# Kernel optimization log

Hardware: AMD Instinct MI355X
Metric: run time of the kernel (lower is better)

The kernel has to match this reference:

```python
import jax, jax.numpy as jnp
import numpy as np

NUM_HEAD = 16


def setup_inputs() -> dict:
    key = jax.random.key(0)
    ks = jax.random.split(key, 7)
    B, S, E = 2, 2048, 1024
    scale = 0.02
    return {
        "x": jax.random.normal(ks[0], (B, S, E), dtype=jnp.float32),
        "Wq": jax.random.normal(ks[1], (E, E), dtype=jnp.float32) * scale,
        "bq": jax.random.normal(ks[2], (E,), dtype=jnp.float32) * scale,
        "Wk": jax.random.normal(ks[3], (E, E), dtype=jnp.float32) * scale,
        "bk": jax.random.normal(ks[4], (E,), dtype=jnp.float32) * scale,
        "Wv": jax.random.normal(ks[5], (E, E), dtype=jnp.float32) * scale,
        "bv": jax.random.normal(ks[6], (E,), dtype=jnp.float32) * scale,
    }


def reference(x, Wq, bq, Wk, bk, Wv, bv):
    B, S, E = x.shape
    H = NUM_HEAD
    Dh = E // H
    # torch Linear: y = x @ W.T + b
    q = (x @ Wq.T + bq).reshape(B, S, H, Dh).transpose(0, 2, 1, 3)  # [B,H,S,Dh]
    k = (x @ Wk.T + bk).reshape(B, S, H, Dh).transpose(0, 2, 1, 3)
    v = (x @ Wv.T + bv).reshape(B, S, H, Dh).transpose(0, 2, 1, 3)
    attn = jnp.einsum("bhqd,bhkd->bhqk", q, k) / jnp.sqrt(jnp.float32(Dh))
    score = jax.nn.softmax(attn, axis=-1)
    out = jnp.einsum("bhqk,bhkd->bhqd", score, v)  # [B,H,S,Dh]
    return out.transpose(0, 2, 1, 3).reshape(B, S, E)
```

## Files before the change

### kernel.cpp

```cpp
#include <hip/hip_runtime.h>
#include <hip/hip_bf16.h>
#include <stdint.h>

#define S_LEN 2048
#define E_DIM 1024
#define NHEAD 16
#define DHEAD 64
#define BATCH 2

typedef short bf16x8 __attribute__((ext_vector_type(8)));
typedef float f32x4 __attribute__((ext_vector_type(4)));
typedef float f32x16 __attribute__((ext_vector_type(16)));

__device__ __forceinline__ ushort f2bf(float f) {
    uint32_t u = __builtin_bit_cast(uint32_t, f);
    u += 0x7fffu + ((u >> 16) & 1u);
    return (ushort)(u >> 16);
}
__device__ __forceinline__ float bf2f(ushort h) {
    uint32_t u = ((uint32_t)h) << 16;
    return __builtin_bit_cast(float, u);
}
__device__ __forceinline__ uint32_t packbf2(float a, float b) {
    return (uint32_t)f2bf(a) | ((uint32_t)f2bf(b) << 16);
}
__device__ __forceinline__ f32x16 zero16() {
    f32x16 v;
    #pragma unroll
    for (int i = 0; i < 16; ++i) v[i] = 0.f;
    return v;
}

__global__ __launch_bounds__(256) void convert_kernel(
    const float* __restrict__ x, const float* __restrict__ wq,
    const float* __restrict__ wk, const float* __restrict__ wv,
    ushort* __restrict__ xb, ushort* __restrict__ wqb,
    ushort* __restrict__ wkb, ushort* __restrict__ wvb)
{
    const int a = blockIdx.y;
    const float* src = (a == 0) ? x : (a == 1) ? wq : (a == 2) ? wk : wv;
    ushort* dst      = (a == 0) ? xb : (a == 1) ? wqb : (a == 2) ? wkb : wvb;
    const int n4 = (a == 0) ? (BATCH * S_LEN * E_DIM / 4) : (E_DIM * E_DIM / 4);
    const int idx = blockIdx.x * 256 + threadIdx.x;
    if (idx < n4) {
        float4 v = reinterpret_cast<const float4*>(src)[idx];
        ushort4 o;
        o.x = f2bf(v.x); o.y = f2bf(v.y); o.z = f2bf(v.z); o.w = f2bf(v.w);
        reinterpret_cast<ushort4*>(dst)[idx] = o;
    }
}

__global__ __launch_bounds__(256) void qkv_mfma_kernel(
    const ushort* __restrict__ xb, const ushort* __restrict__ wqb,
    const ushort* __restrict__ wkb, const ushort* __restrict__ wvb,
    const float* __restrict__ bq, const float* __restrict__ bk,
    const float* __restrict__ bv,
    ushort* __restrict__ qb, ushort* __restrict__ kb, ushort* __restrict__ vtb)
{
    const int z = blockIdx.z;
    const ushort* Ag; const ushort* Bg; const float* bias;
    int m0, n0;
    if (z == 2) { Ag = wvb; Bg = xb;                 bias = bv;
                  m0 = blockIdx.y * 128; n0 = blockIdx.x * 128; }
    else        { Ag = xb;  Bg = (z == 0) ? wqb : wkb; bias = (z == 0) ? bq : bk;
                  m0 = blockIdx.x * 128; n0 = blockIdx.y * 128; }

    __shared__ ushort As[128 * 32];
    __shared__ ushort Bs[128 * 32];

    const int tid  = threadIdx.x;
    const int lane = tid & 63;
    const int wid  = tid >> 6;
    const int wr   = wid >> 1, wc = wid & 1;

    f32x4 acc[4][4];
    #pragma unroll
    for (int i = 0; i < 4; ++i)
        #pragma unroll
        for (int j = 0; j < 4; ++j) acc[i][j] = (f32x4){0.f, 0.f, 0.f, 0.f};

    const int srow0 = tid >> 2;
    const int scol  = (tid & 3) * 8;
    const int lr    = lane & 15;
    const int lc    = (lane >> 4) * 8;

    for (int k0 = 0; k0 < E_DIM; k0 += 32) {
        #pragma unroll
        for (int p = 0; p < 2; ++p) {
            const int row = srow0 + p * 64;
            bf16x8 av = *reinterpret_cast<const bf16x8*>(
                &Ag[(size_t)(m0 + row) * E_DIM + k0 + scol]);
            bf16x8 bv8 = *reinterpret_cast<const bf16x8*>(
                &Bg[(size_t)(n0 + row) * E_DIM + k0 + scol]);
            const int sw = scol ^ (((row >> 1) & 3) << 3);
            *reinterpret_cast<bf16x8*>(&As[row * 32 + sw]) = av;
            *reinterpret_cast<bf16x8*>(&Bs[row * 32 + sw]) = bv8;
        }
        __syncthreads();

        bf16x8 af[4], bf[4];
        #pragma unroll
        for (int mi = 0; mi < 4; ++mi) {
            const int row = wr * 64 + mi * 16 + lr;
            af[mi] = *reinterpret_cast<const bf16x8*>(
                &As[row * 32 + (lc ^ (((row >> 1) & 3) << 3))]);
        }
        #pragma unroll
        for (int ni = 0; ni < 4; ++ni) {
            const int row = wc * 64 + ni * 16 + lr;
            bf[ni] = *reinterpret_cast<const bf16x8*>(
                &Bs[row * 32 + (lc ^ (((row >> 1) & 3) << 3))]);
        }
        #pragma unroll
        for (int mi = 0; mi < 4; ++mi)
            #pragma unroll
            for (int ni = 0; ni < 4; ++ni)
                acc[mi][ni] = __builtin_amdgcn_mfma_f32_16x16x32_bf16(
                    af[mi], bf[ni], acc[mi][ni], 0, 0, 0);
        __syncthreads();
    }

    const int rq = lane >> 4;
    #pragma unroll
    for (int mi = 0; mi < 4; ++mi) {
        #pragma unroll
        for (int ni = 0; ni < 4; ++ni) {
            #pragma unroll
            for (int r = 0; r < 4; ++r) {
                const int i = m0 + wr * 64 + mi * 16 + rq * 4 + r;
                const int j = n0 + wc * 64 + ni * 16 + lr;
                float val = acc[mi][ni][r];
                if (z == 2) {
                    val += bias[i];
                    const int h = i >> 6, d = i & 63;
                    const int b = j >> 11, s = j & (S_LEN - 1);
                    vtb[(((size_t)(b * NHEAD + h)) * DHEAD + d) * S_LEN + s] = f2bf(val);
                } else {
                    val += bias[j];
                    const int h = j >> 6, d = j & 63;
                    const int b = i >> 11, s = i & (S_LEN - 1);
                    ushort* o = (z == 0) ? qb : kb;
                    o[(((size_t)(b * NHEAD + h)) * S_LEN + s) * DHEAD + d] = f2bf(val);
                }
            }
        }
    }
}

__global__ __launch_bounds__(256) void attn_mfma32_kernel(
    const ushort* __restrict__ qb, const ushort* __restrict__ kb,
    const ushort* __restrict__ vtb, float* __restrict__ out)
{
    const int bid = blockIdx.x;
    const int swzb = (bid & 7) * 64 + (bid >> 3);
    const int bh = swzb >> 4;
    const int q0 = (swzb & 15) * 128;
    const int b = bh >> 4, h = bh & 15;
    const ushort* Q  = qb  + (size_t)bh * S_LEN * DHEAD;
    const ushort* K  = kb  + (size_t)bh * S_LEN * DHEAD;
    const ushort* Vt = vtb + (size_t)bh * DHEAD * S_LEN;

    __shared__ ushort smem[128 * 64];
    ushort* Ks = smem;
    ushort* Vs = smem + 64 * 64;

    const int tid  = threadIdx.x;
    const int lane = tid & 63;
    const int wid  = tid >> 6;
    const int hi   = lane >> 5;
    const int l31  = lane & 31;
    const int swzr = (lane & 7) << 3;
    const float CSCALE = 0.125f * 1.4426950408889634f;

    {
        const int slot = (tid & 7) * 8;
        #pragma unroll
        for (int p = 0; p < 4; ++p) {
            const int row = (tid >> 3) + p * 32;
            bf16x8 v = *reinterpret_cast<const bf16x8*>(
                &Q[(size_t)(q0 + row) * DHEAD + slot]);
            *reinterpret_cast<bf16x8*>(
                &smem[row * 64 + (slot ^ ((row & 7) << 3))]) = v;
        }
    }
    __syncthreads();

    bf16x8 qf[4];
    {
        const int qrow = wid * 32 + l31;
        #pragma unroll
        for (int st = 0; st < 4; ++st)
            qf[st] = *reinterpret_cast<const bf16x8*>(
                &smem[qrow * 64 + ((st * 16 + hi * 8) ^ swzr)]);
    }

    float m_run = -1e30f, l_run = 0.f;
    f32x16 oacc[2] = {zero16(), zero16()};

    const int stslot = (tid & 7) * 8;
    const int strow  = tid >> 3;

    for (int t0 = 0; t0 < S_LEN; t0 += 64) {
        __syncthreads();
        #pragma unroll
        for (int p = 0; p < 2; ++p) {
            const int row = strow + p * 32;
            const int sw  = row * 64 + (stslot ^ ((row & 7) << 3));
            bf16x8 kv8 = *reinterpret_cast<const bf16x8*>(
                &K[(size_t)(t0 + row) * DHEAD + stslot]);
            bf16x8 vv8 = *reinterpret_cast<const bf16x8*>(
                &Vt[(size_t)row * S_LEN + t0 + stslot]);
            *reinterpret_cast<bf16x8*>(&Ks[sw]) = kv8;
            *reinterpret_cast<bf16x8*>(&Vs[sw]) = vv8;
        }
        __syncthreads();

        f32x16 sacc[2] = {zero16(), zero16()};
        #pragma unroll
        for (int t = 0; t < 2; ++t) {
            const int kbase = (t * 32 + l31) * 64;
            #pragma unroll
            for (int st = 0; st < 4; ++st) {
                bf16x8 kf = *reinterpret_cast<const bf16x8*>(
                    &Ks[kbase + ((st * 16 + hi * 8) ^ swzr)]);
                sacc[t] = __builtin_amdgcn_mfma_f32_32x32x16_bf16(
                    kf, qf[st], sacc[t], 0, 0, 0);
            }
        }

        float mx = sacc[0][0];
        #pragma unroll
        for (int r = 1; r < 16; ++r) mx = fmaxf(mx, sacc[0][r]);
        #pragma unroll
        for (int r = 0; r < 16; ++r) mx = fmaxf(mx, sacc[1][r]);
        mx = fmaxf(mx, __shfl_xor(mx, 32));
        const float mt = mx * CSCALE;

        if (__any(mt > m_run + 8.0f)) {
            const float mn = fmaxf(m_run, mt);
            const float al = exp2f(m_run - mn);
            m_run = mn;
            l_run *= al;
            #pragma unroll
            for (int r = 0; r < 16; ++r) { oacc[0][r] *= al; oacc[1][r] *= al; }
        }

        float lsum = 0.f;
        uint32_t w[4][4];
        #pragma unroll
        for (int t = 0; t < 2; ++t) {
            #pragma unroll
            for (int half = 0; half < 2; ++half) {
                float p[8];
                #pragma unroll
                for (int j = 0; j < 8; ++j) {
                    p[j] = exp2f(fmaf(sacc[t][half * 8 + j], CSCALE, -m_run));
                    lsum += p[j];
                }
                const uint32_t a0 = packbf2(p[0], p[1]);
                const uint32_t a1 = packbf2(p[2], p[3]);
                const uint32_t b0 = packbf2(p[4], p[5]);
                const uint32_t b1 = packbf2(p[6], p[7]);
                const uint32_t xs0 = __shfl_xor(a0, 32);
                const uint32_t ys0 = __shfl_xor(b0, 32);
                const uint32_t xs1 = __shfl_xor(a1, 32);
                const uint32_t ys1 = __shfl_xor(b1, 32);
                const int c = t * 2 + half;
                w[c][0] = hi ? ys0 : a0;
                w[c][2] = hi ? b0  : xs0;
                w[c][1] = hi ? ys1 : a1;
                w[c][3] = hi ? b1  : xs1;
            }
        }
        lsum += __shfl_xor(lsum, 32);
        l_run += lsum;

        #pragma unroll
        for (int c = 0; c < 4; ++c) {
            union { uint32_t u[4]; bf16x8 v; } pf;
            pf.u[0] = w[c][0]; pf.u[1] = w[c][1];
            pf.u[2] = w[c][2]; pf.u[3] = w[c][3];
            #pragma unroll
            for (int dblk = 0; dblk < 2; ++dblk) {
                const int vrow = dblk * 32 + l31;
                bf16x8 vf = *reinterpret_cast<const bf16x8*>(
                    &Vs[vrow * 64 + ((c * 16 + hi * 8) ^ swzr)]);
                oacc[dblk] = __builtin_amdgcn_mfma_f32_32x32x16_bf16(
                    vf, pf.v, oacc[dblk], 0, 0, 0);
            }
        }
    }

    const float inv = 1.f / l_run;
    const int qg = q0 + wid * 32 + l31;
    float* obase = &out[((size_t)(b * S_LEN + qg)) * E_DIM + h * DHEAD];
    #pragma unroll
    for (int dblk = 0; dblk < 2; ++dblk) {
        #pragma unroll
        for (int g = 0; g < 4; ++g) {
            float4 f;
            f.x = oacc[dblk][g * 4 + 0] * inv;
            f.y = oacc[dblk][g * 4 + 1] * inv;
            f.z = oacc[dblk][g * 4 + 2] * inv;
            f.w = oacc[dblk][g * 4 + 3] * inv;
            *reinterpret_cast<float4*>(&obase[dblk * 32 + g * 8 + hi * 4]) = f;
        }
    }
}

extern "C" void kernel_launch(void* const* d_in, const int* in_sizes, int n_in,
                              void* d_out, int out_size, void* d_ws, size_t ws_size,
                              hipStream_t stream) {
    const float* x  = (const float*)d_in[0];
    const float* Wq = (const float*)d_in[1];
    const float* bq = (const float*)d_in[2];
    const float* Wk = (const float*)d_in[3];
    const float* bk = (const float*)d_in[4];
    const float* Wv = (const float*)d_in[5];
    const float* bv = (const float*)d_in[6];
    float* out = (float*)d_out;

    const size_t XN = (size_t)BATCH * S_LEN * E_DIM;
    const size_t WN = (size_t)E_DIM * E_DIM;
    ushort* xb  = (ushort*)d_ws;
    ushort* wqb = xb  + XN;
    ushort* wkb = wqb + WN;
    ushort* wvb = wkb + WN;
    ushort* qbb = wvb + WN;
    ushort* kbb = qbb + XN;
    ushort* vtb = kbb + XN;

    convert_kernel<<<dim3(4096, 4), 256, 0, stream>>>(
        x, Wq, Wk, Wv, xb, wqb, wkb, wvb);

    qkv_mfma_kernel<<<dim3(32, 8, 3), 256, 0, stream>>>(
        xb, wqb, wkb, wvb, bq, bk, bv, qbb, kbb, vtb);

    attn_mfma32_kernel<<<dim3(512), 256, 0, stream>>>(qbb, kbb, vtb, out);
}
```

Baseline: 212.7 us.

## Double-buffer K/V tiles in attention, use direct-to-LDS loads in GEMM

The attention kernel now prefetches the next K/V tile into registers while computing on the current tile, then writes it into a second LDS buffer, so global load latency overlaps with MFMA and softmax work. The GEMM staging switches to global_load_lds (direct global-to-LDS 16-byte loads), which drops the XOR swizzle and the register round trip. The P-to-bf16 packing uses the hardware v_cvt_pk_bf16_f32 instruction in place of manual rounding. Costs: more LDS per attention block (lower occupancy), and possible LDS bank conflicts in the now unswizzled GEMM tiles.

```diff
diff --git a/kernel.cpp b/kernel.cpp
--- a/kernel.cpp
+++ b/kernel.cpp
@@ -17,18 +17,21 @@
     u += 0x7fffu + ((u >> 16) & 1u);
     return (ushort)(u >> 16);
 }
-__device__ __forceinline__ float bf2f(ushort h) {
-    uint32_t u = ((uint32_t)h) << 16;
-    return __builtin_bit_cast(float, u);
-}
-__device__ __forceinline__ uint32_t packbf2(float a, float b) {
-    return (uint32_t)f2bf(a) | ((uint32_t)f2bf(b) << 16);
+__device__ __forceinline__ uint32_t cvtpk(float lo, float hi) {
+    uint32_t r;
+    asm("v_cvt_pk_bf16_f32 %0, %1, %2" : "=v"(r) : "v"(lo), "v"(hi));
+    return r;
 }
 __device__ __forceinline__ f32x16 zero16() {
     f32x16 v;
     #pragma unroll
     for (int i = 0; i < 16; ++i) v[i] = 0.f;
     return v;
+}
+__device__ __forceinline__ void gload16(const void* g, void* l) {
+    __builtin_amdgcn_global_load_lds(
+        (const __attribute__((address_space(1))) uint32_t*)g,
+        (__attribute__((address_space(3))) uint32_t*)l, 16, 0, 0);
 }
 
 __global__ __launch_bounds__(256) void convert_kernel(
@@ -79,38 +82,31 @@
         #pragma unroll
         for (int j = 0; j < 4; ++j) acc[i][j] = (f32x4){0.f, 0.f, 0.f, 0.f};
 
-    const int srow0 = tid >> 2;
-    const int scol  = (tid & 3) * 8;
-    const int lr    = lane & 15;
-    const int lc    = (lane >> 4) * 8;
+    const int grow = lane >> 2;
+    const int gcol = (lane & 3) * 8;
+    const int lr   = lane & 15;
+    const int lc   = (lane >> 4) * 8;
 
     for (int k0 = 0; k0 < E_DIM; k0 += 32) {
         #pragma unroll
-        for (int p = 0; p < 2; ++p) {
-            const int row = srow0 + p * 64;
-            bf16x8 av = *reinterpret_cast<const bf16x8*>(
-                &Ag[(size_t)(m0 + row) * E_DIM + k0 + scol]);
-            bf16x8 bv8 = *reinterpret_cast<const bf16x8*>(
-                &Bg[(size_t)(n0 + row) * E_DIM + k0 + scol]);
-            const int sw = scol ^ (((row >> 1) & 3) << 3);
-            *reinterpret_cast<bf16x8*>(&As[row * 32 + sw]) = av;
-            *reinterpret_cast<bf16x8*>(&Bs[row * 32 + sw]) = bv8;
+        for (int j = 0; j < 2; ++j) {
+            const int rbase = wid * 32 + j * 16;
+            gload16(&Ag[(size_t)(m0 + rbase + grow) * E_DIM + k0 + gcol],
+                    &As[rbase * 32]);
+            gload16(&Bg[(size_t)(n0 + rbase + grow) * E_DIM + k0 + gcol],
+                    &Bs[rbase * 32]);
         }
         __syncthreads();
 
         bf16x8 af[4], bf[4];
         #pragma unroll
-        for (int mi = 0; mi < 4; ++mi) {
-            const int row = wr * 64 + mi * 16 + lr;
+        for (int mi = 0; mi < 4; ++mi)
             af[mi] = *reinterpret_cast<const bf16x8*>(
-                &As[row * 32 + (lc ^ (((row >> 1) & 3) << 3))]);
-        }
-        #pragma unroll
-        for (int ni = 0; ni < 4; ++ni) {
-            const int row = wc * 64 + ni * 16 + lr;
+                &As[(wr * 64 + mi * 16 + lr) * 32 + lc]);
+        #pragma unroll
+        for (int ni = 0; ni < 4; ++ni)
             bf[ni] = *reinterpret_cast<const bf16x8*>(
-                &Bs[row * 32 + (lc ^ (((row >> 1) & 3) << 3))]);
-        }
+                &Bs[(wc * 64 + ni * 16 + lr) * 32 + lc]);
         #pragma unroll
         for (int mi = 0; mi < 4; ++mi)
             #pragma unroll
@@ -160,9 +156,8 @@
     const ushort* K  = kb  + (size_t)bh * S_LEN * DHEAD;
     const ushort* Vt = vtb + (size_t)bh * DHEAD * S_LEN;
 
-    __shared__ ushort smem[128 * 64];
-    ushort* Ks = smem;
-    ushort* Vs = smem + 64 * 64;
+    __shared__ ushort Qs[128 * 64];
+    __shared__ ushort KV[2][2 * 64 * 64];
 
     const int tid  = threadIdx.x;
     const int lane = tid & 63;
@@ -172,6 +167,9 @@
     const int swzr = (lane & 7) << 3;
     const float CSCALE = 0.125f * 1.4426950408889634f;
 
+    const int stslot = (tid & 7) * 8;
+    const int strow  = tid >> 3;
+
     {
         const int slot = (tid & 7) * 8;
         #pragma unroll
@@ -180,8 +178,18 @@
             bf16x8 v = *reinterpret_cast<const bf16x8*>(
                 &Q[(size_t)(q0 + row) * DHEAD + slot]);
             *reinterpret_cast<bf16x8*>(
-                &smem[row * 64 + (slot ^ ((row & 7) << 3))]) = v;
-        }
+                &Qs[row * 64 + (slot ^ ((row & 7) << 3))]) = v;
+        }
+    }
+
+    bf16x8 kreg[2], vreg[2];
+    #pragma unroll
+    for (int p = 0; p < 2; ++p) {
+        const int row = strow + p * 32;
+        kreg[p] = *reinterpret_cast<const bf16x8*>(
+            &K[(size_t)row * DHEAD + stslot]);
+        vreg[p] = *reinterpret_cast<const bf16x8*>(
+            &Vt[(size_t)row * S_LEN + stslot]);
     }
     __syncthreads();
 
@@ -191,29 +199,38 @@
         #pragma unroll
         for (int st = 0; st < 4; ++st)
             qf[st] = *reinterpret_cast<const bf16x8*>(
-                &smem[qrow * 64 + ((st * 16 + hi * 8) ^ swzr)]);
-    }
+                &Qs[qrow * 64 + ((st * 16 + hi * 8) ^ swzr)]);
+    }
+
+    #pragma unroll
+    for (int p = 0; p < 2; ++p) {
+        const int row = strow + p * 32;
+        const int sw  = row * 64 + (stslot ^ ((row & 7) << 3));
+        *reinterpret_cast<bf16x8*>(&KV[0][sw])           = kreg[p];
+        *reinterpret_cast<bf16x8*>(&KV[0][64 * 64 + sw]) = vreg[p];
+    }
+    __syncthreads();
 
     float m_run = -1e30f, l_run = 0.f;
     f32x16 oacc[2] = {zero16(), zero16()};
-
-    const int stslot = (tid & 7) * 8;
-    const int strow  = tid >> 3;
+    int cur = 0;
 
     for (int t0 = 0; t0 < S_LEN; t0 += 64) {
-        __syncthreads();
-        #pragma unroll
-        for (int p = 0; p < 2; ++p) {
-            const int row = strow + p * 32;
-            const int sw  = row * 64 + (stslot ^ ((row & 7) << 3));
-            bf16x8 kv8 = *reinterpret_cast<const bf16x8*>(
-                &K[(size_t)(t0 + row) * DHEAD + stslot]);
-            bf16x8 vv8 = *reinterpret_cast<const bf16x8*>(
-                &Vt[(size_t)row * S_LEN + t0 + stslot]);
-            *reinterpret_cast<bf16x8*>(&Ks[sw]) = kv8;
-            *reinterpret_cast<bf16x8*>(&Vs[sw]) = vv8;
-        }
-        __syncthreads();
+        const bool more = (t0 + 64 < S_LEN);
+        if (more) {
+            const int tn = t0 + 64;
+            #pragma unroll
+            for (int p = 0; p < 2; ++p) {
+                const int row = strow + p * 32;
+                kreg[p] = *reinterpret_cast<const bf16x8*>(
+                    &K[(size_t)(tn + row) * DHEAD + stslot]);
+                vreg[p] = *reinterpret_cast<const bf16x8*>(
+                    &Vt[(size_t)row * S_LEN + tn + stslot]);
+            }
+        }
+
+        const ushort* Ks = &KV[cur][0];
+        const ushort* Vs = &KV[cur][64 * 64];
 
         f32x16 sacc[2] = {zero16(), zero16()};
         #pragma unroll
@@ -257,10 +274,10 @@
                     p[j] = exp2f(fmaf(sacc[t][half * 8 + j], CSCALE, -m_run));
                     lsum += p[j];
                 }
-                const uint32_t a0 = packbf2(p[0], p[1]);
-                const uint32_t a1 = packbf2(p[2], p[3]);
-                const uint32_t b0 = packbf2(p[4], p[5]);
-                const uint32_t b1 = packbf2(p[6], p[7]);
+                const uint32_t a0 = cvtpk(p[0], p[1]);
+                const uint32_t a1 = cvtpk(p[2], p[3]);
+                const uint32_t b0 = cvtpk(p[4], p[5]);
+                const uint32_t b1 = cvtpk(p[6], p[7]);
                 const uint32_t xs0 = __shfl_xor(a0, 32);
                 const uint32_t ys0 = __shfl_xor(b0, 32);
                 const uint32_t xs1 = __shfl_xor(a1, 32);
@@ -288,6 +305,19 @@
                 oacc[dblk] = __builtin_amdgcn_mfma_f32_32x32x16_bf16(
                     vf, pf.v, oacc[dblk], 0, 0, 0);
             }
+        }
+
+        if (more) {
+            __syncthreads();
+            #pragma unroll
+            for (int p = 0; p < 2; ++p) {
+                const int row = strow + p * 32;
+                const int sw  = row * 64 + (stslot ^ ((row & 7) << 3));
+                *reinterpret_cast<bf16x8*>(&KV[cur ^ 1][sw])           = kreg[p];
+                *reinterpret_cast<bf16x8*>(&KV[cur ^ 1][64 * 64 + sw]) = vreg[p];
+            }
+            __syncthreads();
+            cur ^= 1;
         }
     }
 
```

Measured after the change: 195.4 us. -8.1%, faster.
